# Optimization experiments

Hardware: AMD Instinct MI355X
Metric: run time of the kernel (lower is better)

Reference implementation:

```python
import jax, jax.numpy as jnp
import numpy as np

BN_EPS = 1e-5


def setup_inputs() -> dict:
    key = jax.random.key(0)
    ks = jax.random.split(key, 8)
    bs, N, J, F_in, F_out = 8, 1024, 3, 32, 64
    num_inputs = J * F_in          # 96
    h1 = F_out // 2                # fc1 out
    h2 = F_out - h1                # fc2 out
    WW = jax.random.normal(ks[0], (bs, N, N, J), dtype=jnp.float32)
    x = jax.random.normal(ks[1], (bs, N, F_in), dtype=jnp.float32)
    s = 1.0 / np.sqrt(num_inputs)
    W1 = jax.random.uniform(ks[2], (h1, num_inputs), minval=-s, maxval=s, dtype=jnp.float32)
    b1 = jax.random.uniform(ks[3], (h1,), minval=-s, maxval=s, dtype=jnp.float32)
    W2 = jax.random.uniform(ks[4], (h2, num_inputs), minval=-s, maxval=s, dtype=jnp.float32)
    b2 = jax.random.uniform(ks[5], (h2,), minval=-s, maxval=s, dtype=jnp.float32)
    gamma = jnp.ones((F_out,), dtype=jnp.float32)
    beta = jnp.zeros((F_out,), dtype=jnp.float32)
    return {"WW": WW, "x": x, "W1": W1, "b1": b1, "W2": W2, "b2": b2,
            "gamma": gamma, "beta": beta}


def reference(WW, x, W1, b1, W2, b2, gamma, beta):
    bs, N, _, J = WW.shape
    # GMul: split/cat/bmm chain is equivalent to a single einsum.
    # out[b,n,j,f] = sum_m W[b,n,m,j] * x[b,m,f]; cat order -> (bs, N, J*F)
    y = jnp.einsum('bnmj,bmf->bnjf', WW, x).reshape(bs * N, J * x.shape[-1])
    x1 = jax.nn.relu(y @ W1.T + b1)
    x2 = y @ W2.T + b2
    z = jnp.concatenate([x1, x2], axis=1)           # (bs*N, F_out)
    # BatchNorm1d in training mode: biased batch statistics over bs*N rows
    mean = jnp.mean(z, axis=0)
    var = jnp.var(z, axis=0)
    z = (z - mean) * jax.lax.rsqrt(var + BN_EPS) * gamma + beta
    return z.reshape(bs, N, -1)
```

## Files before the change

### kernel.cpp

```cpp
#include <hip/hip_runtime.h>

typedef __attribute__((ext_vector_type(8))) short bh8;
typedef __attribute__((ext_vector_type(4))) float fx4;

__device__ __forceinline__ unsigned short f2bf(float f) {
  unsigned u = __float_as_uint(f);
  u += 0x7FFFu + ((u >> 16) & 1u);
  return (unsigned short)(u >> 16);
}

__device__ __forceinline__ void async_g2l16(const void* g, void* l) {
  __builtin_amdgcn_global_load_lds(
      (const __attribute__((address_space(1))) unsigned int*)g,
      (__attribute__((address_space(3))) unsigned int*)l, 16, 0, 0);
}

__global__ void __launch_bounds__(256) k0_bt(const float* __restrict__ x,
    const float* __restrict__ W1, const float* __restrict__ W2,
    unsigned short* __restrict__ bt) {
  __shared__ float xl[64][32];
  __shared__ float wl[96][64];
  int t = threadIdx.x;
  int bid = blockIdx.x;
  int b = bid >> 4, c = bid & 15;

  for (int i = t; i < 6144; i += 256) {
    int k = i >> 6, o = i & 63;
    wl[k][o] = (o < 32) ? W1[o * 96 + k] : W2[(o - 32) * 96 + k];
  }
  const float4* xs = (const float4*)(x + (size_t)(b * 1024 + c * 64) * 32);
  ((float4*)xl)[t]       = xs[t];
  ((float4*)xl)[t + 256] = xs[t + 256];
  __syncthreads();

  int o = t & 63;
  int q = t >> 6;
  unsigned short* orow = bt + (size_t)(b * 64 + o) * 3072;
#pragma unroll 1
  for (int gi = 0; gi < 2; ++gi) {
    int m0 = (q + gi * 4) * 8;
    float acc[8][3];
#pragma unroll
    for (int m = 0; m < 8; ++m) acc[m][0] = acc[m][1] = acc[m][2] = 0.f;
#pragma unroll
    for (int f4 = 0; f4 < 8; ++f4) {
      float wv[3][4];
#pragma unroll
      for (int u = 0; u < 4; ++u) {
        int f = f4 * 4 + u;
        wv[0][u] = wl[f][o];
        wv[1][u] = wl[32 + f][o];
        wv[2][u] = wl[64 + f][o];
      }
#pragma unroll
      for (int m = 0; m < 8; ++m) {
        float4 xv = *(const float4*)&xl[m0 + m][f4 * 4];
#pragma unroll
        for (int j = 0; j < 3; ++j) {
          acc[m][j] = fmaf(xv.x, wv[j][0], acc[m][j]);
          acc[m][j] = fmaf(xv.y, wv[j][1], acc[m][j]);
          acc[m][j] = fmaf(xv.z, wv[j][2], acc[m][j]);
          acc[m][j] = fmaf(xv.w, wv[j][3], acc[m][j]);
        }
      }
    }
    unsigned pk[12];
#pragma unroll
    for (int i = 0; i < 12; ++i) {
      unsigned short lo = f2bf(acc[(2 * i) / 3][(2 * i) % 3]);
      unsigned short hi = f2bf(acc[(2 * i + 1) / 3][(2 * i + 1) % 3]);
      pk[i] = (unsigned)lo | ((unsigned)hi << 16);
    }
    uint4* op = (uint4*)(orow + 3 * (c * 64 + m0));
    op[0] = make_uint4(pk[0], pk[1], pk[2], pk[3]);
    op[1] = make_uint4(pk[4], pk[5], pk[6], pk[7]);
    op[2] = make_uint4(pk[8], pk[9], pk[10], pk[11]);
  }
}

__global__ void __launch_bounds__(256, 8) k1_gemm(const float* __restrict__ A,
    const unsigned short* __restrict__ BT, float* __restrict__ parts) {
  __shared__ __align__(16) unsigned char smem[20480];
  int t = threadIdx.x;
  int w = t >> 6, l = t & 63;
  int bid = blockIdx.x;
  int ks = bid & 3, mt = bid >> 2;
  int r0 = mt * 16;
  int b = mt >> 6;
  const unsigned char* btb = (const unsigned char*)BT + (size_t)b * 393216 + ks * 1536;

  int arow = t >> 4, acol = t & 15;
  const float* aptr = A + (size_t)(r0 + arow) * 3072 + ks * 768 + acol * 4;
  int awoff = arow * 128 + ((acol * 8) ^ ((arow & 7) << 4));

  int lr = l & 15, lg = l >> 4;
  int swz = (lr & 7) << 4;

  fx4 acc = {0.f, 0.f, 0.f, 0.f};
  float4 ra;

  auto stageB = [&](unsigned char* Bn, int koff) {
#pragma unroll
    for (int i = 0; i < 2; ++i) {
      int L = i * 4096 + w * 1024 + l * 16;
      int oo = L >> 7, inrow = L & 127;
      async_g2l16(btb + (size_t)oo * 6144 + koff + (inrow ^ ((oo & 7) << 4)),
                  smem + (Bn - smem) + i * 4096 + w * 1024);
    }
  };
  auto packA = [&](unsigned char* An, float4 v) {
    unsigned p0 = (unsigned)f2bf(v.x) | ((unsigned)f2bf(v.y) << 16);
    unsigned p1 = (unsigned)f2bf(v.z) | ((unsigned)f2bf(v.w) << 16);
    *(uint2*)(An + awoff) = make_uint2(p0, p1);
  };

  stageB(smem + 4096, 0);
  ra = *(const float4*)aptr;
  packA(smem, ra);
  __syncthreads();

#pragma unroll 2
  for (int s = 0; s < 12; ++s) {
    unsigned char* Ac = smem + (s & 1) * 2048;
    unsigned char* Bc = smem + 4096 + (s & 1) * 8192;
    unsigned char* An = smem + ((s + 1) & 1) * 2048;
    unsigned char* Bn = smem + 4096 + ((s + 1) & 1) * 8192;
    if (s < 11) {
      stageB(Bn, (s + 1) * 128);
      ra = *(const float4*)(aptr + (s + 1) * 64);
    }
#pragma unroll
    for (int sub = 0; sub < 2; ++sub) {
      int ko = (sub * 64 + lg * 16) ^ swz;
      bh8 av = *(const bh8*)(Ac + lr * 128 + ko);
      bh8 bv = *(const bh8*)(Bc + (w * 16 + lr) * 128 + ko);
      acc = __builtin_amdgcn_mfma_f32_16x16x32_bf16(av, bv, acc, 0, 0, 0);
    }
    if (s < 11) packA(An, ra);
    __syncthreads();
  }

  float* pout = parts + (size_t)ks * 524288 + (size_t)r0 * 64 + w * 16 + lr;
#pragma unroll
  for (int r = 0; r < 4; ++r)
    pout[(lg * 4 + r) * 64] = acc[r];
}

__global__ void __launch_bounds__(256) k2_red(const float* __restrict__ parts,
    const float* __restrict__ b1, const float* __restrict__ b2,
    float* __restrict__ z, float2* __restrict__ part2) {
  __shared__ float4 redA[4][16], redB[4][16];
  int t = threadIdx.x, bid = blockIdx.x;
  int w = t >> 6, l = t & 63;
  int o0 = (t & 15) * 4;
  float4 bias = (o0 < 32) ? ((const float4*)b1)[o0 >> 2]
                          : ((const float4*)b2)[(o0 - 32) >> 2];
  bool rl = (o0 < 32);
  float4 s1 = {0.f, 0.f, 0.f, 0.f}, s2 = {0.f, 0.f, 0.f, 0.f};
  const float4* p0 = (const float4*)parts;
#pragma unroll
  for (int k = 0; k < 4; ++k) {
    int i4 = bid * 1024 + k * 256 + t;
    float4 v  = p0[i4];
    float4 v1 = p0[131072 + i4];
    float4 v2 = p0[262144 + i4];
    float4 v3 = p0[393216 + i4];
    v.x += v1.x + v2.x + v3.x + bias.x;
    v.y += v1.y + v2.y + v3.y + bias.y;
    v.z += v1.z + v2.z + v3.z + bias.z;
    v.w += v1.w + v2.w + v3.w + bias.w;
    if (rl) {
      v.x = fmaxf(v.x, 0.f); v.y = fmaxf(v.y, 0.f);
      v.z = fmaxf(v.z, 0.f); v.w = fmaxf(v.w, 0.f);
    }
    ((float4*)z)[i4] = v;
    s1.x += v.x; s1.y += v.y; s1.z += v.z; s1.w += v.w;
    s2.x += v.x * v.x; s2.y += v.y * v.y; s2.z += v.z * v.z; s2.w += v.w * v.w;
  }
#define RED_(c) { s1.c += __shfl_xor(s1.c, 16); s1.c += __shfl_xor(s1.c, 32); \
                  s2.c += __shfl_xor(s2.c, 16); s2.c += __shfl_xor(s2.c, 32); }
  RED_(x) RED_(y) RED_(z) RED_(w)
#undef RED_
  if (l < 16) { redA[w][l] = s1; redB[w][l] = s2; }
  __syncthreads();
  if (t < 16) {
    float4 S = redA[0][t], Q = redB[0][t];
#pragma unroll
    for (int wv = 1; wv < 4; ++wv) {
      float4 a = redA[wv][t], q = redB[wv][t];
      S.x += a.x; S.y += a.y; S.z += a.z; S.w += a.w;
      Q.x += q.x; Q.y += q.y; Q.z += q.z; Q.w += q.w;
    }
    int ob = bid * 64 + t * 4;
    part2[ob + 0] = make_float2(S.x, Q.x);
    part2[ob + 1] = make_float2(S.y, Q.y);
    part2[ob + 2] = make_float2(S.z, Q.z);
    part2[ob + 3] = make_float2(S.w, Q.w);
  }
}

__global__ void k3_stats(const float2* __restrict__ part2, const float* __restrict__ gamma,
                         const float* __restrict__ beta, float2* __restrict__ stats) {
  __shared__ float red[2][4][64];
  int t = threadIdx.x;
  int o = t & 63, c = t >> 6;
  float S = 0.f, Q = 0.f;
#pragma unroll 4
  for (int i = 0; i < 32; ++i) {
    float2 p = part2[(c * 32 + i) * 64 + o];
    S += p.x; Q += p.y;
  }
  red[0][c][o] = S; red[1][c][o] = Q;
  __syncthreads();
  if (t < 64) {
    float Ss = 0.f, Qs = 0.f;
#pragma unroll
    for (int cc = 0; cc < 4; ++cc) { Ss += red[0][cc][t]; Qs += red[1][cc][t]; }
    float mean = Ss * (1.0f / 8192.0f);
    float var = fmaxf(Qs * (1.0f / 8192.0f) - mean * mean, 0.f);
    float rstd = rsqrtf(var + 1e-5f);
    float scale = gamma[t] * rstd;
    stats[t] = make_float2(scale, beta[t] - mean * scale);
  }
}

__global__ void k4_norm(float* __restrict__ z, const float2* __restrict__ stats) {
  int i4 = blockIdx.x * 256 + threadIdx.x;
  float4 v = ((const float4*)z)[i4];
  int o0 = (i4 & 15) * 4;
  float2 s0 = stats[o0 + 0], s1 = stats[o0 + 1], s2 = stats[o0 + 2], s3 = stats[o0 + 3];
  v.x = v.x * s0.x + s0.y;
  v.y = v.y * s1.x + s1.y;
  v.z = v.z * s2.x + s2.y;
  v.w = v.w * s3.x + s3.y;
  ((float4*)z)[i4] = v;
}

extern "C" void kernel_launch(void* const* d_in, const int* in_sizes, int n_in,
                              void* d_out, int out_size, void* d_ws, size_t ws_size,
                              hipStream_t stream) {
  const float* WW = (const float*)d_in[0];
  const float* x  = (const float*)d_in[1];
  const float* W1 = (const float*)d_in[2];
  const float* b1 = (const float*)d_in[3];
  const float* W2 = (const float*)d_in[4];
  const float* b2 = (const float*)d_in[5];
  const float* gamma = (const float*)d_in[6];
  const float* beta  = (const float*)d_in[7];

  unsigned short* bt = (unsigned short*)d_ws;
  float*  parts = (float*)((char*)d_ws + 3145728);
  float2* part2 = (float2*)((char*)d_ws + 11534336);
  float2* stats = (float2*)((char*)d_ws + 11599872);
  float* z = (float*)d_out;

  hipLaunchKernelGGL(k0_bt,    dim3(128),  dim3(256), 0, stream, x, W1, W2, bt);
  hipLaunchKernelGGL(k1_gemm,  dim3(2048), dim3(256), 0, stream, WW, bt, parts);
  hipLaunchKernelGGL(k2_red,   dim3(128),  dim3(256), 0, stream, parts, b1, b2, z, part2);
  hipLaunchKernelGGL(k3_stats, dim3(1),    dim3(256), 0, stream, part2, gamma, beta, stats);
  hipLaunchKernelGGL(k4_norm,  dim3(512),  dim3(256), 0, stream, z, stats);
}
```

Baseline: 186.9 us.

## Rewrite GEMM to register-direct loads with 64-row tiles and 8-way split-K

The main GEMM kernel no longer stages A and B through LDS with async loads and barriers. Each wave now loads its A fragment from global memory straight into registers, converts it to bf16, and reuses it across four MFMA column tiles covering all 64 outputs. B fragments also come straight from global, double-buffered in registers. Split-K goes from 4 to 8, which doubles the partial-sum buffer traffic in the reduction kernel, and the precompute kernel now uses more, smaller blocks. The intent is to remove LDS round-trips and syncs, with the risk of less coalesced strided global loads and more partial-sum traffic.

```diff
diff --git a/kernel.cpp b/kernel.cpp
--- a/kernel.cpp
+++ b/kernel.cpp
@@ -9,141 +9,128 @@
   return (unsigned short)(u >> 16);
 }
 
-__device__ __forceinline__ void async_g2l16(const void* g, void* l) {
-  __builtin_amdgcn_global_load_lds(
-      (const __attribute__((address_space(1))) unsigned int*)g,
-      (__attribute__((address_space(3))) unsigned int*)l, 16, 0, 0);
+__device__ __forceinline__ bh8 pack8(float4 u, float4 v) {
+  bh8 r;
+  r[0] = (short)f2bf(u.x); r[1] = (short)f2bf(u.y);
+  r[2] = (short)f2bf(u.z); r[3] = (short)f2bf(u.w);
+  r[4] = (short)f2bf(v.x); r[5] = (short)f2bf(v.y);
+  r[6] = (short)f2bf(v.z); r[7] = (short)f2bf(v.w);
+  return r;
 }
 
 __global__ void __launch_bounds__(256) k0_bt(const float* __restrict__ x,
     const float* __restrict__ W1, const float* __restrict__ W2,
     unsigned short* __restrict__ bt) {
-  __shared__ float xl[64][32];
+  __shared__ float xl[32][32];
   __shared__ float wl[96][64];
   int t = threadIdx.x;
   int bid = blockIdx.x;
-  int b = bid >> 4, c = bid & 15;
-
-  for (int i = t; i < 6144; i += 256) {
-    int k = i >> 6, o = i & 63;
-    wl[k][o] = (o < 32) ? W1[o * 96 + k] : W2[(o - 32) * 96 + k];
-  }
-  const float4* xs = (const float4*)(x + (size_t)(b * 1024 + c * 64) * 32);
-  ((float4*)xl)[t]       = xs[t];
-  ((float4*)xl)[t + 256] = xs[t + 256];
+  int b = bid >> 5, c = bid & 31;
+
+  for (int i = t; i < 3072; i += 256) {
+    int r = i / 96, k = i - r * 96;
+    wl[k][r]      = W1[i];
+    wl[k][r + 32] = W2[i];
+  }
+  const float4* xs = (const float4*)(x + (size_t)(b * 1024 + c * 32) * 32);
+  ((float4*)xl)[t] = xs[t];
   __syncthreads();
 
   int o = t & 63;
   int q = t >> 6;
+  int m0 = q * 8;
+  float acc[8][3];
+#pragma unroll
+  for (int m = 0; m < 8; ++m) acc[m][0] = acc[m][1] = acc[m][2] = 0.f;
+#pragma unroll
+  for (int f4 = 0; f4 < 8; ++f4) {
+    float wv[3][4];
+#pragma unroll
+    for (int u = 0; u < 4; ++u) {
+      int f = f4 * 4 + u;
+      wv[0][u] = wl[f][o];
+      wv[1][u] = wl[32 + f][o];
+      wv[2][u] = wl[64 + f][o];
+    }
+#pragma unroll
+    for (int m = 0; m < 8; ++m) {
+      float4 xv = *(const float4*)&xl[m0 + m][f4 * 4];
+#pragma unroll
+      for (int j = 0; j < 3; ++j) {
+        acc[m][j] = fmaf(xv.x, wv[j][0], acc[m][j]);
+        acc[m][j] = fmaf(xv.y, wv[j][1], acc[m][j]);
+        acc[m][j] = fmaf(xv.z, wv[j][2], acc[m][j]);
+        acc[m][j] = fmaf(xv.w, wv[j][3], acc[m][j]);
+      }
+    }
+  }
+  unsigned pk[12];
+#pragma unroll
+  for (int i = 0; i < 12; ++i) {
+    unsigned short lo = f2bf(acc[(2 * i) / 3][(2 * i) % 3]);
+    unsigned short hi = f2bf(acc[(2 * i + 1) / 3][(2 * i + 1) % 3]);
+    pk[i] = (unsigned)lo | ((unsigned)hi << 16);
+  }
   unsigned short* orow = bt + (size_t)(b * 64 + o) * 3072;
-#pragma unroll 1
-  for (int gi = 0; gi < 2; ++gi) {
-    int m0 = (q + gi * 4) * 8;
-    float acc[8][3];
-#pragma unroll
-    for (int m = 0; m < 8; ++m) acc[m][0] = acc[m][1] = acc[m][2] = 0.f;
-#pragma unroll
-    for (int f4 = 0; f4 < 8; ++f4) {
-      float wv[3][4];
-#pragma unroll
-      for (int u = 0; u < 4; ++u) {
-        int f = f4 * 4 + u;
-        wv[0][u] = wl[f][o];
-        wv[1][u] = wl[32 + f][o];
-        wv[2][u] = wl[64 + f][o];
-      }
-#pragma unroll
-      for (int m = 0; m < 8; ++m) {
-        float4 xv = *(const float4*)&xl[m0 + m][f4 * 4];
-#pragma unroll
-        for (int j = 0; j < 3; ++j) {
-          acc[m][j] = fmaf(xv.x, wv[j][0], acc[m][j]);
-          acc[m][j] = fmaf(xv.y, wv[j][1], acc[m][j]);
-          acc[m][j] = fmaf(xv.z, wv[j][2], acc[m][j]);
-          acc[m][j] = fmaf(xv.w, wv[j][3], acc[m][j]);
-        }
-      }
-    }
-    unsigned pk[12];
-#pragma unroll
-    for (int i = 0; i < 12; ++i) {
-      unsigned short lo = f2bf(acc[(2 * i) / 3][(2 * i) % 3]);
-      unsigned short hi = f2bf(acc[(2 * i + 1) / 3][(2 * i + 1) % 3]);
-      pk[i] = (unsigned)lo | ((unsigned)hi << 16);
-    }
-    uint4* op = (uint4*)(orow + 3 * (c * 64 + m0));
-    op[0] = make_uint4(pk[0], pk[1], pk[2], pk[3]);
-    op[1] = make_uint4(pk[4], pk[5], pk[6], pk[7]);
-    op[2] = make_uint4(pk[8], pk[9], pk[10], pk[11]);
-  }
-}
-
-__global__ void __launch_bounds__(256, 8) k1_gemm(const float* __restrict__ A,
+  uint4* op = (uint4*)(orow + 3 * (c * 32 + m0));
+  op[0] = make_uint4(pk[0], pk[1], pk[2], pk[3]);
+  op[1] = make_uint4(pk[4], pk[5], pk[6], pk[7]);
+  op[2] = make_uint4(pk[8], pk[9], pk[10], pk[11]);
+}
+
+__global__ void __launch_bounds__(256) k1_gemm(const float* __restrict__ A,
     const unsigned short* __restrict__ BT, float* __restrict__ parts) {
-  __shared__ __align__(16) unsigned char smem[20480];
   int t = threadIdx.x;
   int w = t >> 6, l = t & 63;
+  int lr = l & 15, lg = l >> 4;
   int bid = blockIdx.x;
-  int ks = bid & 3, mt = bid >> 2;
-  int r0 = mt * 16;
-  int b = mt >> 6;
-  const unsigned char* btb = (const unsigned char*)BT + (size_t)b * 393216 + ks * 1536;
-
-  int arow = t >> 4, acol = t & 15;
-  const float* aptr = A + (size_t)(r0 + arow) * 3072 + ks * 768 + acol * 4;
-  int awoff = arow * 128 + ((acol * 8) ^ ((arow & 7) << 4));
-
-  int lr = l & 15, lg = l >> 4;
-  int swz = (lr & 7) << 4;
-
-  fx4 acc = {0.f, 0.f, 0.f, 0.f};
-  float4 ra;
-
-  auto stageB = [&](unsigned char* Bn, int koff) {
-#pragma unroll
-    for (int i = 0; i < 2; ++i) {
-      int L = i * 4096 + w * 1024 + l * 16;
-      int oo = L >> 7, inrow = L & 127;
-      async_g2l16(btb + (size_t)oo * 6144 + koff + (inrow ^ ((oo & 7) << 4)),
-                  smem + (Bn - smem) + i * 4096 + w * 1024);
-    }
-  };
-  auto packA = [&](unsigned char* An, float4 v) {
-    unsigned p0 = (unsigned)f2bf(v.x) | ((unsigned)f2bf(v.y) << 16);
-    unsigned p1 = (unsigned)f2bf(v.z) | ((unsigned)f2bf(v.w) << 16);
-    *(uint2*)(An + awoff) = make_uint2(p0, p1);
-  };
-
-  stageB(smem + 4096, 0);
-  ra = *(const float4*)aptr;
-  packA(smem, ra);
-  __syncthreads();
-
-#pragma unroll 2
-  for (int s = 0; s < 12; ++s) {
-    unsigned char* Ac = smem + (s & 1) * 2048;
-    unsigned char* Bc = smem + 4096 + (s & 1) * 8192;
-    unsigned char* An = smem + ((s + 1) & 1) * 2048;
-    unsigned char* Bn = smem + 4096 + ((s + 1) & 1) * 8192;
-    if (s < 11) {
-      stageB(Bn, (s + 1) * 128);
-      ra = *(const float4*)(aptr + (s + 1) * 64);
-    }
-#pragma unroll
-    for (int sub = 0; sub < 2; ++sub) {
-      int ko = (sub * 64 + lg * 16) ^ swz;
-      bh8 av = *(const bh8*)(Ac + lr * 128 + ko);
-      bh8 bv = *(const bh8*)(Bc + (w * 16 + lr) * 128 + ko);
-      acc = __builtin_amdgcn_mfma_f32_16x16x32_bf16(av, bv, acc, 0, 0, 0);
-    }
-    if (s < 11) packA(An, ra);
-    __syncthreads();
-  }
-
-  float* pout = parts + (size_t)ks * 524288 + (size_t)r0 * 64 + w * 16 + lr;
-#pragma unroll
-  for (int r = 0; r < 4; ++r)
-    pout[(lg * 4 + r) * 64] = acc[r];
+  int ks = bid & 7, mt = bid >> 3;
+  int arow = mt * 64 + w * 16 + lr;
+  int b = mt >> 4;
+  int kbase = ks * 384 + lg * 8;
+  const float* ap = A + (size_t)arow * 3072 + kbase;
+  const unsigned short* bp = BT + (size_t)b * 196608 + (size_t)lr * 3072 + kbase;
+
+  fx4 acc0 = {0.f,0.f,0.f,0.f}, acc1 = {0.f,0.f,0.f,0.f};
+  fx4 acc2 = {0.f,0.f,0.f,0.f}, acc3 = {0.f,0.f,0.f,0.f};
+
+#define LOADA_(s, ra, rb) { ra = *(const float4*)(ap + (s) * 32); \
+                            rb = *(const float4*)(ap + (s) * 32 + 4); }
+#define LOADB_(s, c0, c1, c2, c3) { \
+    c0 = *(const bh8*)(bp + (s) * 32); \
+    c1 = *(const bh8*)(bp + 49152 + (s) * 32); \
+    c2 = *(const bh8*)(bp + 98304 + (s) * 32); \
+    c3 = *(const bh8*)(bp + 147456 + (s) * 32); }
+#define STEP_(ra, rb, c0, c1, c2, c3) { bh8 av = pack8(ra, rb); \
+    acc0 = __builtin_amdgcn_mfma_f32_16x16x32_bf16(av, c0, acc0, 0, 0, 0); \
+    acc1 = __builtin_amdgcn_mfma_f32_16x16x32_bf16(av, c1, acc1, 0, 0, 0); \
+    acc2 = __builtin_amdgcn_mfma_f32_16x16x32_bf16(av, c2, acc2, 0, 0, 0); \
+    acc3 = __builtin_amdgcn_mfma_f32_16x16x32_bf16(av, c3, acc3, 0, 0, 0); }
+
+  float4 aA0, aA1, aB0, aB1;
+  bh8 bA0, bA1, bA2, bA3, bB0, bB1, bB2, bB3;
+  LOADA_(0, aA0, aA1); LOADB_(0, bA0, bA1, bA2, bA3);
+  LOADA_(1, aB0, aB1); LOADB_(1, bB0, bB1, bB2, bB3);
+#pragma unroll
+  for (int s = 0; s < 12; s += 2) {
+    STEP_(aA0, aA1, bA0, bA1, bA2, bA3);
+    if (s + 2 < 12) { LOADA_(s + 2, aA0, aA1); LOADB_(s + 2, bA0, bA1, bA2, bA3); }
+    STEP_(aB0, aB1, bB0, bB1, bB2, bB3);
+    if (s + 3 < 12) { LOADA_(s + 3, aB0, aB1); LOADB_(s + 3, bB0, bB1, bB2, bB3); }
+  }
+#undef LOADA_
+#undef LOADB_
+#undef STEP_
+
+  float* pout = parts + ((size_t)ks * 8192 + (size_t)mt * 64 + w * 16) * 64;
+#pragma unroll
+  for (int r = 0; r < 4; ++r) {
+    int ro = (lg * 4 + r) * 64 + lr;
+    pout[ro]      = acc0[r];
+    pout[ro + 16] = acc1[r];
+    pout[ro + 32] = acc2[r];
+    pout[ro + 48] = acc3[r];
+  }
 }
 
 __global__ void __launch_bounds__(256) k2_red(const float* __restrict__ parts,
@@ -159,16 +146,15 @@
   float4 s1 = {0.f, 0.f, 0.f, 0.f}, s2 = {0.f, 0.f, 0.f, 0.f};
   const float4* p0 = (const float4*)parts;
 #pragma unroll
-  for (int k = 0; k < 4; ++k) {
-    int i4 = bid * 1024 + k * 256 + t;
-    float4 v  = p0[i4];
-    float4 v1 = p0[131072 + i4];
-    float4 v2 = p0[262144 + i4];
-    float4 v3 = p0[393216 + i4];
-    v.x += v1.x + v2.x + v3.x + bias.x;
-    v.y += v1.y + v2.y + v3.y + bias.y;
-    v.z += v1.z + v2.z + v3.z + bias.z;
-    v.w += v1.w + v2.w + v3.w + bias.w;
+  for (int kk = 0; kk < 4; ++kk) {
+    int i4 = bid * 1024 + kk * 256 + t;
+    float4 v = p0[i4];
+#pragma unroll
+    for (int j = 1; j < 8; ++j) {
+      float4 vj = p0[j * 131072 + i4];
+      v.x += vj.x; v.y += vj.y; v.z += vj.z; v.w += vj.w;
+    }
+    v.x += bias.x; v.y += bias.y; v.z += bias.z; v.w += bias.w;
     if (rl) {
       v.x = fmaxf(v.x, 0.f); v.y = fmaxf(v.y, 0.f);
       v.z = fmaxf(v.z, 0.f); v.w = fmaxf(v.w, 0.f);
@@ -250,12 +236,12 @@
 
   unsigned short* bt = (unsigned short*)d_ws;
   float*  parts = (float*)((char*)d_ws + 3145728);
-  float2* part2 = (float2*)((char*)d_ws + 11534336);
-  float2* stats = (float2*)((char*)d_ws + 11599872);
+  float2* part2 = (float2*)((char*)d_ws + 3145728 + 16777216);
+  float2* stats = (float2*)((char*)d_ws + 3145728 + 16777216 + 65536);
   float* z = (float*)d_out;
 
-  hipLaunchKernelGGL(k0_bt,    dim3(128),  dim3(256), 0, stream, x, W1, W2, bt);
-  hipLaunchKernelGGL(k1_gemm,  dim3(2048), dim3(256), 0, stream, WW, bt, parts);
+  hipLaunchKernelGGL(k0_bt,    dim3(256),  dim3(256), 0, stream, x, W1, W2, bt);
+  hipLaunchKernelGGL(k1_gemm,  dim3(1024), dim3(256), 0, stream, WW, bt, parts);
   hipLaunchKernelGGL(k2_red,   dim3(128),  dim3(256), 0, stream, parts, b1, b2, z, part2);
   hipLaunchKernelGGL(k3_stats, dim3(1),    dim3(256), 0, stream, part2, gamma, beta, stats);
   hipLaunchKernelGGL(k4_norm,  dim3(512),  dim3(256), 0, stream, z, stats);
```

New measurement: 194.5 us. +4.1%, slower.
